# Performance work log

Measured on AMD Instinct MI355X. Metric: run time of the kernel, lower is better.

The kernel has to match this reference:

```python
import jax, jax.numpy as jnp
import numpy as np
import math

D_MODEL = 1024
N_HEADS = 16
HEAD_DIM = D_MODEL // N_HEADS
B = 2
S = 2048

def setup_inputs() -> dict:
    key = jax.random.key(0)
    ks = jax.random.split(key, 5)
    x = jax.random.normal(ks[0], (B, S, D_MODEL), dtype=jnp.float32)
    # causal lower-triangular mask, broadcastable to [B, H, S, S]
    mask = jnp.tril(jnp.ones((S, S), dtype=bool))[None, None, :, :]
    # qkv_proj: Linear(d_model, 3*d_model); out_proj: Linear(d_model, d_model)
    lim_qkv = 1.0 / math.sqrt(D_MODEL)
    Wqkv = jax.random.uniform(ks[1], (D_MODEL, 3 * D_MODEL), minval=-lim_qkv, maxval=lim_qkv, dtype=jnp.float32)
    bqkv = jax.random.uniform(ks[2], (3 * D_MODEL,), minval=-lim_qkv, maxval=lim_qkv, dtype=jnp.float32)
    Wo = jax.random.uniform(ks[3], (D_MODEL, D_MODEL), minval=-lim_qkv, maxval=lim_qkv, dtype=jnp.float32)
    bo = jax.random.uniform(ks[4], (D_MODEL,), minval=-lim_qkv, maxval=lim_qkv, dtype=jnp.float32)
    return {"x": x, "mask": mask, "Wqkv": Wqkv, "bqkv": bqkv, "Wo": Wo, "bo": bo}

def reference(x, mask, Wqkv, bqkv, Wo, bo):
    b, s, d = x.shape
    scale = math.sqrt(HEAD_DIM)
    qkv = x @ Wqkv + bqkv                                   # [b, s, 3d]
    qkv = qkv.reshape(b, s, 3, N_HEADS, HEAD_DIM)
    qkv = jnp.transpose(qkv, (2, 0, 3, 1, 4))               # [3, b, h, s, hd]
    q, k, v = qkv[0], qkv[1], qkv[2]
    scores = jnp.einsum("bhqd,bhkd->bhqk", q, k) / scale    # [b, h, s, s]
    scores = jnp.where(mask, scores, -jnp.inf)
    attn = jax.nn.softmax(scores, axis=-1)                  # dropout inactive (eval)
    out = jnp.einsum("bhqk,bhkd->bhqd", attn, v)            # [b, h, s, hd]
    out = jnp.transpose(out, (0, 2, 1, 3)).reshape(b, s, d)
    return out @ Wo + bo
```

## Files before the change

kernel.cpp:

```cpp
#include <hip/hip_runtime.h>
#include <stdint.h>

typedef __bf16 bf16x8 __attribute__((ext_vector_type(8)));
typedef float  f32x4  __attribute__((ext_vector_type(4)));

__device__ __forceinline__ float bf2f(ushort u) {
    union { uint i; float f; } v; v.i = ((uint)u) << 16; return v.f;
}
__device__ __forceinline__ ushort f2bf(float f) {
    union { uint i; float f; } v; v.f = f;
    uint i = v.i;
    uint r = (i + 0x7fffu + ((i >> 16) & 1u)) >> 16;
    return (ushort)r;
}
__device__ __forceinline__ ushort f2bf_t(float f) {
    union { uint i; float f; } v; v.f = f;
    return (ushort)(v.i >> 16);
}

__device__ __forceinline__ void gld16(const ushort* g, ushort* l) {
    __builtin_amdgcn_global_load_lds((const __attribute__((address_space(1))) uint*)g,
                                     (__attribute__((address_space(3))) uint*)l, 16, 0, 0);
}

#define D_MODEL 1024
#define N_HEADS 16
#define HEAD_DIM 64
#define BATCH 2
#define SEQ 2048
#define M_ROWS (BATCH * SEQ)
#define SCALE_LOG2E 0.18033688f
#define N_ITEMS 768

__global__ __launch_bounds__(256) void cast_f32_bf16(
    const float* __restrict__ in, ushort* __restrict__ out, int n4)
{
    int i = blockIdx.x * 256 + threadIdx.x;
    if (i < n4) {
        float4 v = ((const float4*)in)[i];
        ushort4 o;
        o.x = f2bf(v.x); o.y = f2bf(v.y); o.z = f2bf(v.z); o.w = f2bf(v.w);
        ((ushort4*)out)[i] = o;
    }
}

__global__ __launch_bounds__(256) void transpose_f32_bf16(
    const float* __restrict__ in, ushort* __restrict__ out, int K, int N)
{
    __shared__ float tile[64][65];
    const int k0 = blockIdx.y << 6, n0 = blockIdx.x << 6;
    const int tid = threadIdx.x;
    {
        const int r  = tid >> 4;
        const int c4 = (tid & 15) * 4;
#pragma unroll
        for (int rr = 0; rr < 4; ++rr) {
            int kk = r + rr * 16;
            float4 v = *(const float4*)(in + (size_t)(k0 + kk) * N + n0 + c4);
            tile[kk][c4 + 0] = v.x; tile[kk][c4 + 1] = v.y;
            tile[kk][c4 + 2] = v.z; tile[kk][c4 + 3] = v.w;
        }
    }
    __syncthreads();
    {
        const int nn = tid & 63;
        const int ch = tid >> 6;
#pragma unroll
        for (int cc = 0; cc < 2; ++cc) {
            int k8 = (ch + cc * 4) * 8;
            ushort tmp[8] __attribute__((aligned(16)));
#pragma unroll
            for (int j = 0; j < 8; ++j) tmp[j] = f2bf(tile[k8 + j][nn]);
            *(uint4*)(out + (size_t)(n0 + nn) * K + k0 + k8) = *(const uint4*)tmp;
        }
    }
}

__global__ __launch_bounds__(256) void gemm_bt128(
    const ushort* __restrict__ A, const ushort* __restrict__ Bt,
    const float* __restrict__ bias, float* __restrict__ out,
    ushort* __restrict__ Qb, ushort* __restrict__ Kb, ushort* __restrict__ Vb,
    int M, int N, int K, int mode)
{
    __shared__ ushort As[128 * 32];
    __shared__ ushort Bs[128 * 32];
    const int tid = threadIdx.x, lane = tid & 63, w = tid >> 6;
    const int wr = w >> 1, wc = w & 1;
    const int m0 = blockIdx.y * 128, n0 = blockIdx.x * 128;
    const int quad = lane >> 4, r15 = lane & 15, q8 = quad * 8;

    f32x4 acc[4][4] = {};

    const int cb0 = w * 64;
    const int cb1 = 256 + w * 64;
    const int c0 = cb0 + lane, c1 = cb1 + lane;
    const int row0 = c0 >> 2, sc0 = (c0 & 3) * 8;
    const int row1 = c1 >> 2, sc1 = (c1 & 3) * 8;

    for (int k0 = 0; k0 < K; k0 += 32) {
        gld16(A  + (size_t)(m0 + row0) * K + k0 + sc0, As + cb0 * 8);
        gld16(A  + (size_t)(m0 + row1) * K + k0 + sc1, As + cb1 * 8);
        gld16(Bt + (size_t)(n0 + row0) * K + k0 + sc0, Bs + cb0 * 8);
        gld16(Bt + (size_t)(n0 + row1) * K + k0 + sc1, Bs + cb1 * 8);
        __syncthreads();
        bf16x8 af[4], bfv[4];
#pragma unroll
        for (int mt = 0; mt < 4; ++mt)
            af[mt] = *(const bf16x8*)&As[(wr * 64 + mt * 16 + r15) * 32 + q8];
#pragma unroll
        for (int nt = 0; nt < 4; ++nt)
            bfv[nt] = *(const bf16x8*)&Bs[(wc * 64 + nt * 16 + r15) * 32 + q8];
#pragma unroll
        for (int mt = 0; mt < 4; ++mt)
#pragma unroll
            for (int nt = 0; nt < 4; ++nt)
                acc[mt][nt] = __builtin_amdgcn_mfma_f32_16x16x32_bf16(af[mt], bfv[nt], acc[mt][nt], 0, 0, 0);
        __syncthreads();
    }

    const int q4 = quad * 4;
    float bv[4];
#pragma unroll
    for (int nt = 0; nt < 4; ++nt) bv[nt] = bias[n0 + wc * 64 + nt * 16 + r15];
#pragma unroll
    for (int mt = 0; mt < 4; ++mt) {
#pragma unroll
        for (int nt = 0; nt < 4; ++nt) {
#pragma unroll
            for (int r = 0; r < 4; ++r) {
                int m = m0 + wr * 64 + mt * 16 + q4 + r;
                int n = n0 + wc * 64 + nt * 16 + r15;
                float v = acc[mt][nt][r] + bv[nt];
                if (mode == 0) {
                    int which = n >> 10, nh = n & 1023;
                    int h = nh >> 6, d = nh & 63;
                    int b = m >> 11, s = m & 2047;
                    size_t dst = (((size_t)(b * N_HEADS + h)) * SEQ + s) * HEAD_DIM + d;
                    ushort* p = (which == 0) ? Qb : ((which == 1) ? Kb : Vb);
                    p[dst] = f2bf(v);
                } else {
                    out[(size_t)m * N + n] = v;
                }
            }
        }
    }
}

__global__ __launch_bounds__(512, 4) void attn_mfma(
    const ushort* __restrict__ Q, const ushort* __restrict__ K,
    const ushort* __restrict__ V, ushort* __restrict__ Out,
    float* __restrict__ Opart, float* __restrict__ lpart,
    int* __restrict__ counter)
{
    __shared__ ushort Ks[2][64 * 72];
    __shared__ ushort Vt[2][64 * 72];
    __shared__ ushort Ps[8][16 * 72];
    __shared__ int s_item;

    const int tid  = threadIdx.x;
    const int lane = tid & 63;
    const int w    = tid >> 6;
    const int quad = lane >> 4;
    const int r15  = lane & 15;
    const int q8   = quad * 8;

    const int srow = tid >> 3;
    const int scol = (tid & 7) * 8;
    const int kp = tid & 31;
    const int dg = tid >> 5;

    for (;;) {
        __syncthreads();
        if (tid == 0) s_item = atomicAdd(counter, 1);
        __syncthreads();
        const int item = s_item;
        if (item >= N_ITEMS) break;

        int p, bh, t0, t1, half;
        if (item < 512) {
            p = 15 - (item >> 6);
            half = (item >> 5) & 1;
            bh = item & 31;
            const int hl = p + 1;
            t0 = half * hl; t1 = t0 + hl;
        } else {
            const int j = item - 512;
            p = 7 - (j >> 5);
            bh = j & 31;
            half = -1;
            t0 = 0; t1 = 2 * p + 2;
        }
        const int ntf  = 2 * p + 2;
        const int q0   = p * 128;
        const int wq0  = q0 + w * 16;
        const int tdiag = ntf - 2 + (w >> 2);
        const size_t base = (size_t)bh * SEQ * HEAD_DIM;

        bf16x8 qf[2];
        {
            const ushort* qrow = Q + base + (size_t)(wq0 + r15) * HEAD_DIM;
            qf[0] = *(const bf16x8*)(qrow + q8);
            qf[1] = *(const bf16x8*)(qrow + 32 + q8);
        }

        f32x4 o_acc[4] = {};
        float l_lane[4] = {0.f, 0.f, 0.f, 0.f};

        uint4 kr; uint2 va, vb;
        {
            const int key0 = t0 << 6;
            const ushort* kpt = K + base + (size_t)(key0 + srow) * HEAD_DIM + scol;
            kr = *(const uint4*)kpt;
            const ushort* vpt = V + base + (size_t)(key0 + 2 * kp) * HEAD_DIM + dg * 4;
            va = *(const uint2*)vpt; vb = *(const uint2*)(vpt + HEAD_DIM);
        }
        {
            ushort* ks = &Ks[t0 & 1][0];
            *(uint4*)&ks[srow * 72 + scol] = kr;
            const ushort* ap = (const ushort*)&va;
            const ushort* bp = (const ushort*)&vb;
            uint* vt32 = (uint*)&Vt[t0 & 1][0];
#pragma unroll
            for (int j = 0; j < 4; ++j)
                vt32[(dg * 4 + j) * 36 + kp] = (uint)ap[j] | ((uint)bp[j] << 16);
        }
        if (t0 + 1 < t1) {
            const int key0 = (t0 + 1) << 6;
            const ushort* kpt = K + base + (size_t)(key0 + srow) * HEAD_DIM + scol;
            kr = *(const uint4*)kpt;
            const ushort* vpt = V + base + (size_t)(key0 + 2 * kp) * HEAD_DIM + dg * 4;
            va = *(const uint2*)vpt; vb = *(const uint2*)(vpt + HEAD_DIM);
        }

        for (int t = t0; t < t1; ++t) {
            __syncthreads();
            if (t + 1 < t1) {
                const int b1 = (t + 1) & 1;
                ushort* ks = &Ks[b1][0];
                *(uint4*)&ks[srow * 72 + scol] = kr;
                const ushort* ap = (const ushort*)&va;
                const ushort* bp = (const ushort*)&vb;
                uint* vt32 = (uint*)&Vt[b1][0];
#pragma unroll
                for (int j = 0; j < 4; ++j)
                    vt32[(dg * 4 + j) * 36 + kp] = (uint)ap[j] | ((uint)bp[j] << 16);
            }
            if (t + 2 < t1) {
                const int key2 = (t + 2) << 6;
                const ushort* kpt = K + base + (size_t)(key2 + srow) * HEAD_DIM + scol;
                kr = *(const uint4*)kpt;
                const ushort* vpt = V + base + (size_t)(key2 + 2 * kp) * HEAD_DIM + dg * 4;
                va = *(const uint2*)vpt; vb = *(const uint2*)(vpt + HEAD_DIM);
            }

            const int ntmax = (t < tdiag) ? 4 : ((t == tdiag) ? (w & 3) + 1 : 0);
            if (ntmax == 0) continue;

            const ushort* KsB = &Ks[t & 1][0];
            const ushort* VtB = &Vt[t & 1][0];
            const bool diag = (t == tdiag);

            f32x4 s_acc[4];
#pragma unroll
            for (int nt = 0; nt < 4; ++nt) {
                if (nt >= ntmax) continue;
                f32x4 z = {};
#pragma unroll
                for (int ks = 0; ks < 2; ++ks) {
                    bf16x8 kf = *(const bf16x8*)&KsB[(nt * 16 + r15) * 72 + ks * 32 + q8];
                    z = __builtin_amdgcn_mfma_f32_16x16x32_bf16(qf[ks], kf, z, 0, 0, 0);
                }
                s_acc[nt] = z;
            }
#pragma unroll
            for (int nt = 0; nt < 4; ++nt) {
                if (nt >= ntmax) continue;
#pragma unroll
                for (int j = 0; j < 4; ++j) {
                    float e = exp2f(s_acc[nt][j] * SCALE_LOG2E);
                    if (diag && nt == (w & 3) && r15 > quad * 4 + j) e = 0.f;
                    s_acc[nt][j] = e;
                    l_lane[j] += e;
                }
            }
            ushort* pb = &Ps[w][0];
#pragma unroll
            for (int nt = 0; nt < 4; ++nt)
#pragma unroll
                for (int j = 0; j < 4; ++j)
                    pb[(quad * 4 + j) * 72 + nt * 16 + r15] =
                        (nt < ntmax) ? f2bf_t(s_acc[nt][j]) : (ushort)0;
            bf16x8 pf0 = *(const bf16x8*)&pb[r15 * 72 + q8];
            bf16x8 pf1 = *(const bf16x8*)&pb[r15 * 72 + 32 + q8];

#pragma unroll
            for (int nt = 0; nt < 4; ++nt) {
                const int d0 = nt * 16 + r15;
                bf16x8 vf0 = *(const bf16x8*)&VtB[d0 * 72 + q8];
                bf16x8 vf1 = *(const bf16x8*)&VtB[d0 * 72 + 32 + q8];
                o_acc[nt] = __builtin_amdgcn_mfma_f32_16x16x32_bf16(pf0, vf0, o_acc[nt], 0, 0, 0);
                o_acc[nt] = __builtin_amdgcn_mfma_f32_16x16x32_bf16(pf1, vf1, o_acc[nt], 0, 0, 0);
            }
        }

        float lsum[4];
#pragma unroll
        for (int j = 0; j < 4; ++j) {
            float l = l_lane[j];
            l += __shfl_xor(l, 1);
            l += __shfl_xor(l, 2);
            l += __shfl_xor(l, 4);
            l += __shfl_xor(l, 8);
            lsum[j] = l;
        }
        if (half < 0) {
            const int b = bh >> 4, h = bh & 15;
#pragma unroll
            for (int nt = 0; nt < 4; ++nt) {
#pragma unroll
                for (int j = 0; j < 4; ++j) {
                    int qg = wq0 + quad * 4 + j;
                    float v = o_acc[nt][j] / lsum[j];
                    Out[((size_t)(b * SEQ + qg)) * D_MODEL + h * 64 + nt * 16 + r15] = f2bf(v);
                }
            }
        } else {
            const int qrb = wq0 - 1024;
            float* Ob = Opart + ((size_t)(half * 32 + bh) * 1024) * 64;
#pragma unroll
            for (int nt = 0; nt < 4; ++nt)
#pragma unroll
                for (int j = 0; j < 4; ++j)
                    Ob[(size_t)(qrb + quad * 4 + j) * 64 + nt * 16 + r15] = o_acc[nt][j];
            if (r15 == 0) {
                float* lb = lpart + (size_t)(half * 32 + bh) * 1024;
#pragma unroll
                for (int j = 0; j < 4; ++j)
                    lb[qrb + quad * 4 + j] = lsum[j];
            }
        }
    }
}

__global__ __launch_bounds__(256) void attn_combine(
    const float* __restrict__ Opart, const float* __restrict__ lpart,
    ushort* __restrict__ Out)
{
    const int idx = blockIdx.x * 256 + threadIdx.x;
    const int bh = idx >> 14;
    const int rem = idx & 16383;
    const int qrel = rem >> 4, d4 = (rem & 15) * 4;
    const size_t o0 = ((size_t)bh * 1024 + qrel) * 64 + d4;
    const size_t o1 = ((size_t)(32 + bh) * 1024 + qrel) * 64 + d4;
    float4 a = *(const float4*)(Opart + o0);
    float4 c = *(const float4*)(Opart + o1);
    float l = lpart[bh * 1024 + qrel] + lpart[32 * 1024 + bh * 1024 + qrel];
    float inv = 1.f / l;
    ushort4 r;
    r.x = f2bf((a.x + c.x) * inv);
    r.y = f2bf((a.y + c.y) * inv);
    r.z = f2bf((a.z + c.z) * inv);
    r.w = f2bf((a.w + c.w) * inv);
    const int b = bh >> 4, h = bh & 15;
    *(ushort4*)(Out + ((size_t)(b * SEQ + 1024 + qrel)) * D_MODEL + h * 64 + d4) = r;
}

extern "C" void kernel_launch(void* const* d_in, const int* in_sizes, int n_in,
                              void* d_out, int out_size, void* d_ws, size_t ws_size,
                              hipStream_t stream)
{
    const float* x    = (const float*)d_in[0];
    const float* Wqkv = (const float*)d_in[2];
    const float* bqkv = (const float*)d_in[3];
    const float* Wo   = (const float*)d_in[4];
    const float* bo   = (const float*)d_in[5];
    float* out = (float*)d_out;

    char* ws = (char*)d_ws;
    size_t off = 0;
    ushort* xb    = (ushort*)(ws + off); off += (size_t)M_ROWS * D_MODEL * 2;
    ushort* WqkvT = (ushort*)(ws + off); off += (size_t)3 * D_MODEL * D_MODEL * 2;
    ushort* WoT   = (ushort*)(ws + off); off += (size_t)D_MODEL * D_MODEL * 2;
    const size_t qkv_elems = (size_t)BATCH * N_HEADS * SEQ * HEAD_DIM;
    ushort* Qb = (ushort*)(ws + off); off += qkv_elems * 2;
    ushort* Kb = (ushort*)(ws + off); off += qkv_elems * 2;
    ushort* Vb = (ushort*)(ws + off); off += qkv_elems * 2;
    ushort* attn_out = (ushort*)(ws + off); off += (size_t)M_ROWS * D_MODEL * 2;
    float* Opart = (float*)(ws + off); off += (size_t)2 * 32 * 1024 * 64 * 4;
    float* lpart = (float*)(ws + off); off += (size_t)2 * 32 * 1024 * 4;
    int* counter = (int*)(ws + off); off += 256;

    hipMemsetAsync(counter, 0, 4, stream);

    {
        int n4 = M_ROWS * D_MODEL / 4;
        cast_f32_bf16<<<(n4 + 255) / 256, 256, 0, stream>>>(x, xb, n4);
    }

    transpose_f32_bf16<<<dim3(3 * D_MODEL / 64, D_MODEL / 64), 256, 0, stream>>>(Wqkv, WqkvT, D_MODEL, 3 * D_MODEL);
    transpose_f32_bf16<<<dim3(D_MODEL / 64, D_MODEL / 64), 256, 0, stream>>>(Wo, WoT, D_MODEL, D_MODEL);

    gemm_bt128<<<dim3(3 * D_MODEL / 128, M_ROWS / 128), 256, 0, stream>>>(
        xb, WqkvT, bqkv, nullptr, Qb, Kb, Vb, M_ROWS, 3 * D_MODEL, D_MODEL, 0);

    attn_mfma<<<512, 512, 0, stream>>>(Qb, Kb, Vb, attn_out, Opart, lpart, counter);

    attn_combine<<<2048, 256, 0, stream>>>(Opart, lpart, attn_out);

    gemm_bt128<<<dim3(D_MODEL / 128, M_ROWS / 128), 256, 0, stream>>>(
        attn_out, WoT, bo, out, nullptr, nullptr, nullptr, M_ROWS, D_MODEL, D_MODEL, 1);
}
```

Before: 247.1 us.

## Fuse prep kernels and fold split-KV combine into output projection GEMM

Merges the x cast and both weight transposes into one launch, specialises the QKV GEMM, and removes the attn_combine kernel. The output GEMM now combines the two partial attention results and normalises them while loading its A tile for the second half of each sequence, using 64-row tiles. This saves kernel launches and one write-then-read of the combined attention output. In exchange, the heavy tiles do scalar float loads and conversions in the GEMM inner loop, and each Opart row is reread by every N-block, so that load becomes redundant.

Result: faster. 240.8 us (-2.6%).

```diff
diff --git a/kernel.cpp b/kernel.cpp
--- a/kernel.cpp
+++ b/kernel.cpp
@@ -32,24 +32,35 @@
 #define SCALE_LOG2E 0.18033688f
 #define N_ITEMS 768
 
-__global__ __launch_bounds__(256) void cast_f32_bf16(
-    const float* __restrict__ in, ushort* __restrict__ out, int n4)
+__global__ __launch_bounds__(256) void prep_fused(
+    const float* __restrict__ x, ushort* __restrict__ xb,
+    const float* __restrict__ Wqkv, ushort* __restrict__ WqkvT,
+    const float* __restrict__ Wo, ushort* __restrict__ WoT)
 {
-    int i = blockIdx.x * 256 + threadIdx.x;
-    if (i < n4) {
-        float4 v = ((const float4*)in)[i];
+    __shared__ float tile[64][65];
+    const int blk = blockIdx.x;
+    const int tid = threadIdx.x;
+
+    if (blk < 4096) {
+        int i = blk * 256 + tid;
+        float4 v = ((const float4*)x)[i];
         ushort4 o;
         o.x = f2bf(v.x); o.y = f2bf(v.y); o.z = f2bf(v.z); o.w = f2bf(v.w);
-        ((ushort4*)out)[i] = o;
-    }
-}
-
-__global__ __launch_bounds__(256) void transpose_f32_bf16(
-    const float* __restrict__ in, ushort* __restrict__ out, int K, int N)
-{
-    __shared__ float tile[64][65];
-    const int k0 = blockIdx.y << 6, n0 = blockIdx.x << 6;
-    const int tid = threadIdx.x;
+        ((ushort4*)xb)[i] = o;
+        return;
+    }
+
+    const float* in; ushort* out; int K, N, bx, by;
+    if (blk < 4096 + 768) {
+        int j = blk - 4096;
+        in = Wqkv; out = WqkvT; K = 1024; N = 3072;
+        bx = j % 48; by = j / 48;
+    } else {
+        int j = blk - 4864;
+        in = Wo; out = WoT; K = 1024; N = 1024;
+        bx = j & 15; by = j >> 4;
+    }
+    const int k0 = by << 6, n0 = bx << 6;
     {
         const int r  = tid >> 4;
         const int c4 = (tid & 15) * 4;
@@ -76,11 +87,10 @@
     }
 }
 
-__global__ __launch_bounds__(256) void gemm_bt128(
+__global__ __launch_bounds__(256) void gemm_qkv(
     const ushort* __restrict__ A, const ushort* __restrict__ Bt,
-    const float* __restrict__ bias, float* __restrict__ out,
-    ushort* __restrict__ Qb, ushort* __restrict__ Kb, ushort* __restrict__ Vb,
-    int M, int N, int K, int mode)
+    const float* __restrict__ bias,
+    ushort* __restrict__ Qb, ushort* __restrict__ Kb, ushort* __restrict__ Vb)
 {
     __shared__ ushort As[128 * 32];
     __shared__ ushort Bs[128 * 32];
@@ -88,6 +98,7 @@
     const int wr = w >> 1, wc = w & 1;
     const int m0 = blockIdx.y * 128, n0 = blockIdx.x * 128;
     const int quad = lane >> 4, r15 = lane & 15, q8 = quad * 8;
+    const int K = D_MODEL;
 
     f32x4 acc[4][4] = {};
 
@@ -131,16 +142,12 @@
                 int m = m0 + wr * 64 + mt * 16 + q4 + r;
                 int n = n0 + wc * 64 + nt * 16 + r15;
                 float v = acc[mt][nt][r] + bv[nt];
-                if (mode == 0) {
-                    int which = n >> 10, nh = n & 1023;
-                    int h = nh >> 6, d = nh & 63;
-                    int b = m >> 11, s = m & 2047;
-                    size_t dst = (((size_t)(b * N_HEADS + h)) * SEQ + s) * HEAD_DIM + d;
-                    ushort* p = (which == 0) ? Qb : ((which == 1) ? Kb : Vb);
-                    p[dst] = f2bf(v);
-                } else {
-                    out[(size_t)m * N + n] = v;
-                }
+                int which = n >> 10, nh = n & 1023;
+                int h = nh >> 6, d = nh & 63;
+                int b = m >> 11, s = m & 2047;
+                size_t dst = (((size_t)(b * N_HEADS + h)) * SEQ + s) * HEAD_DIM + d;
+                ushort* p = (which == 0) ? Qb : ((which == 1) ? Kb : Vb);
+                p[dst] = f2bf(v);
             }
         }
     }
@@ -342,27 +349,98 @@
     }
 }
 
-__global__ __launch_bounds__(256) void attn_combine(
+__global__ __launch_bounds__(256) void gemm_out(
+    const ushort* __restrict__ A,
     const float* __restrict__ Opart, const float* __restrict__ lpart,
-    ushort* __restrict__ Out)
+    const ushort* __restrict__ Bt,
+    const float* __restrict__ bias, float* __restrict__ out)
 {
-    const int idx = blockIdx.x * 256 + threadIdx.x;
-    const int bh = idx >> 14;
-    const int rem = idx & 16383;
-    const int qrel = rem >> 4, d4 = (rem & 15) * 4;
-    const size_t o0 = ((size_t)bh * 1024 + qrel) * 64 + d4;
-    const size_t o1 = ((size_t)(32 + bh) * 1024 + qrel) * 64 + d4;
-    float4 a = *(const float4*)(Opart + o0);
-    float4 c = *(const float4*)(Opart + o1);
-    float l = lpart[bh * 1024 + qrel] + lpart[32 * 1024 + bh * 1024 + qrel];
-    float inv = 1.f / l;
-    ushort4 r;
-    r.x = f2bf((a.x + c.x) * inv);
-    r.y = f2bf((a.y + c.y) * inv);
-    r.z = f2bf((a.z + c.z) * inv);
-    r.w = f2bf((a.w + c.w) * inv);
-    const int b = bh >> 4, h = bh & 15;
-    *(ushort4*)(Out + ((size_t)(b * SEQ + 1024 + qrel)) * D_MODEL + h * 64 + d4) = r;
+    __shared__ ushort As[64 * 32];
+    __shared__ ushort Bs[128 * 32];
+    const int tid = threadIdx.x, lane = tid & 63, w = tid >> 6;
+    const int wr = w >> 1, wc = w & 1;
+    const int m0 = blockIdx.y * 64, n0 = blockIdx.x * 128;
+    const int quad = lane >> 4, r15 = lane & 15, q8 = quad * 8;
+    const bool heavy = ((m0 >> 10) & 1) != 0;
+
+    f32x4 acc[2][4] = {};
+
+    const int ca = w * 64 + lane;
+    const int rowa = ca >> 2, sca = (ca & 3) * 8;
+    const int hrow = tid >> 2, hc8 = (tid & 3) * 8;
+    const int m_h = m0 + hrow;
+    const int qrel = (m_h & 2047) - 1024;
+    const int b_h = m_h >> 11;
+    float inv_l = 0.f;
+    if (heavy) {
+    }
+    const int cb0 = w * 64, cb1 = 256 + w * 64;
+    const int c0 = cb0 + lane, c1 = cb1 + lane;
+    const int rowb0 = c0 >> 2, scb0 = (c0 & 3) * 8;
+    const int rowb1 = c1 >> 2, scb1 = (c1 & 3) * 8;
+
+    int cur_h = -1;
+    for (int k0 = 0; k0 < D_MODEL; k0 += 32) {
+        if (heavy) {
+            const int h = k0 >> 6;
+            const int bh = b_h * 16 + h;
+            if (h != cur_h) {
+                float l = lpart[bh * 1024 + qrel] + lpart[32768 + bh * 1024 + qrel];
+                inv_l = 1.f / l;
+                cur_h = h;
+            }
+            const int d = (k0 & 63) + hc8;
+            const float* p0 = Opart + ((size_t)bh * 1024 + qrel) * 64 + d;
+            const float* p1 = p0 + (size_t)32 * 1024 * 64;
+            float4 a0 = *(const float4*)p0, a1 = *(const float4*)(p0 + 4);
+            float4 c0v = *(const float4*)p1, c1v = *(const float4*)(p1 + 4);
+            ushort tmp[8] __attribute__((aligned(16)));
+            tmp[0] = f2bf((a0.x + c0v.x) * inv_l);
+            tmp[1] = f2bf((a0.y + c0v.y) * inv_l);
+            tmp[2] = f2bf((a0.z + c0v.z) * inv_l);
+            tmp[3] = f2bf((a0.w + c0v.w) * inv_l);
+            tmp[4] = f2bf((a1.x + c1v.x) * inv_l);
+            tmp[5] = f2bf((a1.y + c1v.y) * inv_l);
+            tmp[6] = f2bf((a1.z + c1v.z) * inv_l);
+            tmp[7] = f2bf((a1.w + c1v.w) * inv_l);
+            *(uint4*)&As[hrow * 32 + hc8] = *(const uint4*)tmp;
+        } else {
+            gld16(A + (size_t)(m0 + rowa) * D_MODEL + k0 + sca, As + cb0 * 8);
+        }
+        gld16(Bt + (size_t)(n0 + rowb0) * D_MODEL + k0 + scb0, Bs + cb0 * 8);
+        gld16(Bt + (size_t)(n0 + rowb1) * D_MODEL + k0 + scb1, Bs + cb1 * 8);
+        __syncthreads();
+        bf16x8 af[2], bfv[4];
+#pragma unroll
+        for (int mt = 0; mt < 2; ++mt)
+            af[mt] = *(const bf16x8*)&As[(wr * 32 + mt * 16 + r15) * 32 + q8];
+#pragma unroll
+        for (int nt = 0; nt < 4; ++nt)
+            bfv[nt] = *(const bf16x8*)&Bs[(wc * 64 + nt * 16 + r15) * 32 + q8];
+#pragma unroll
+        for (int mt = 0; mt < 2; ++mt)
+#pragma unroll
+            for (int nt = 0; nt < 4; ++nt)
+                acc[mt][nt] = __builtin_amdgcn_mfma_f32_16x16x32_bf16(af[mt], bfv[nt], acc[mt][nt], 0, 0, 0);
+        __syncthreads();
+    }
+
+    const int q4 = quad * 4;
+    float bv[4];
+#pragma unroll
+    for (int nt = 0; nt < 4; ++nt) bv[nt] = bias[n0 + wc * 64 + nt * 16 + r15];
+#pragma unroll
+    for (int mt = 0; mt < 2; ++mt) {
+#pragma unroll
+        for (int nt = 0; nt < 4; ++nt) {
+#pragma unroll
+            for (int r = 0; r < 4; ++r) {
+                int m = m0 + wr * 32 + mt * 16 + q4 + r;
+                int n = n0 + wc * 64 + nt * 16 + r15;
+                out[(size_t)m * D_MODEL + n] = acc[mt][nt][r] + bv[nt];
+            }
+        }
+    }
 }
 
 extern "C" void kernel_launch(void* const* d_in, const int* in_sizes, int n_in,
@@ -392,21 +470,13 @@
 
     hipMemsetAsync(counter, 0, 4, stream);
 
-    {
-        int n4 = M_ROWS * D_MODEL / 4;
-        cast_f32_bf16<<<(n4 + 255) / 256, 256, 0, stream>>>(x, xb, n4);
-    }
-
-    transpose_f32_bf16<<<dim3(3 * D_MODEL / 64, D_MODEL / 64), 256, 0, stream>>>(Wqkv, WqkvT, D_MODEL, 3 * D_MODEL);
-    transpose_f32_bf16<<<dim3(D_MODEL / 64, D_MODEL / 64), 256, 0, stream>>>(Wo, WoT, D_MODEL, D_MODEL);
-
-    gemm_bt128<<<dim3(3 * D_MODEL / 128, M_ROWS / 128), 256, 0, stream>>>(
-        xb, WqkvT, bqkv, nullptr, Qb, Kb, Vb, M_ROWS, 3 * D_MODEL, D_MODEL, 0);
+    prep_fused<<<5120, 256, 0, stream>>>(x, xb, Wqkv, WqkvT, Wo, WoT);
+
+    gemm_qkv<<<dim3(3 * D_MODEL / 128, M_ROWS / 128), 256, 0, stream>>>(
+        xb, WqkvT, bqkv, Qb, Kb, Vb);
 
     attn_mfma<<<512, 512, 0, stream>>>(Qb, Kb, Vb, attn_out, Opart, lpart, counter);
 
-    attn_combine<<<2048, 256, 0, stream>>>(Opart, lpart, attn_out);
-
-    gemm_bt128<<<dim3(D_MODEL / 128, M_ROWS / 128), 256, 0, stream>>>(
-        attn_out, WoT, bo, out, nullptr, nullptr, nullptr, M_ROWS, D_MODEL, D_MODEL, 1);
-}
+    gemm_out<<<dim3(D_MODEL / 128, M_ROWS / 64), 256, 0, stream>>>(
+        attn_out, Opart, lpart, WoT, bo, out);
+}
```

## Fuse whole attention pipeline into one persistent kernel with grid barriers

Applied to the files above, without the earlier changes.

Replaces the seven separate launches (cast, two transposes, QKV GEMM, attention, combine, output GEMM) with a single persistent 256-block kernel whose phases are separated by atomic-counter grid barriers. QKV is now written row-major to one buffer instead of being scattered per head, and attention is statically balanced by pairing a long and a short query block per block, which removes the split-half partial outputs and the combine pass. Launch overhead and the extra partial-output traffic go away, but the GEMMs now run with smaller tiles over only 256 blocks. The grid barriers rely on every block being co-resident and add spin-wait stalls between phases.

After: 362.7 us. 1.47x slower.

```diff
diff --git a/kernel.cpp b/kernel.cpp
--- a/kernel.cpp
+++ b/kernel.cpp
@@ -4,9 +4,6 @@
 typedef __bf16 bf16x8 __attribute__((ext_vector_type(8)));
 typedef float  f32x4  __attribute__((ext_vector_type(4)));
 
-__device__ __forceinline__ float bf2f(ushort u) {
-    union { uint i; float f; } v; v.i = ((uint)u) << 16; return v.f;
-}
 __device__ __forceinline__ ushort f2bf(float f) {
     union { uint i; float f; } v; v.f = f;
     uint i = v.i;
@@ -29,340 +26,320 @@
 #define BATCH 2
 #define SEQ 2048
 #define M_ROWS (BATCH * SEQ)
+#define QKV_W  3072
 #define SCALE_LOG2E 0.18033688f
-#define N_ITEMS 768
-
-__global__ __launch_bounds__(256) void cast_f32_bf16(
-    const float* __restrict__ in, ushort* __restrict__ out, int n4)
+#define NBLK 256
+
+__device__ __forceinline__ void grid_barrier(int* cnt, int target, int tid) {
+    __syncthreads();
+    if (tid == 0) {
+        __threadfence();
+        atomicAdd(cnt, 1);
+        while (__hip_atomic_load(cnt, __ATOMIC_ACQUIRE, __HIP_MEMORY_SCOPE_AGENT) < target)
+            __builtin_amdgcn_s_sleep(2);
+        __threadfence();
+    }
+    __syncthreads();
+}
+
+__global__ __launch_bounds__(512, 4) void fused_all(
+    const float* __restrict__ x,    ushort* __restrict__ xb,
+    const float* __restrict__ Wqkv, ushort* __restrict__ WqkvT,
+    const float* __restrict__ Wo,   ushort* __restrict__ WoT,
+    const float* __restrict__ bqkv, ushort* __restrict__ xqkv,
+    ushort* __restrict__ aout, const float* __restrict__ bo,
+    float* __restrict__ out, int* __restrict__ cnt)
 {
-    int i = blockIdx.x * 256 + threadIdx.x;
-    if (i < n4) {
-        float4 v = ((const float4*)in)[i];
-        ushort4 o;
-        o.x = f2bf(v.x); o.y = f2bf(v.y); o.z = f2bf(v.z); o.w = f2bf(v.w);
-        ((ushort4*)out)[i] = o;
-    }
-}
-
-__global__ __launch_bounds__(256) void transpose_f32_bf16(
-    const float* __restrict__ in, ushort* __restrict__ out, int K, int N)
-{
-    __shared__ float tile[64][65];
-    const int k0 = blockIdx.y << 6, n0 = blockIdx.x << 6;
-    const int tid = threadIdx.x;
-    {
-        const int r  = tid >> 4;
-        const int c4 = (tid & 15) * 4;
-#pragma unroll
-        for (int rr = 0; rr < 4; ++rr) {
-            int kk = r + rr * 16;
-            float4 v = *(const float4*)(in + (size_t)(k0 + kk) * N + n0 + c4);
-            tile[kk][c4 + 0] = v.x; tile[kk][c4 + 1] = v.y;
-            tile[kk][c4 + 2] = v.z; tile[kk][c4 + 3] = v.w;
-        }
-    }
-    __syncthreads();
-    {
-        const int nn = tid & 63;
-        const int ch = tid >> 6;
-#pragma unroll
-        for (int cc = 0; cc < 2; ++cc) {
-            int k8 = (ch + cc * 4) * 8;
-            ushort tmp[8] __attribute__((aligned(16)));
-#pragma unroll
-            for (int j = 0; j < 8; ++j) tmp[j] = f2bf(tile[k8 + j][nn]);
-            *(uint4*)(out + (size_t)(n0 + nn) * K + k0 + k8) = *(const uint4*)tmp;
-        }
-    }
-}
-
-__global__ __launch_bounds__(256) void gemm_bt128(
-    const ushort* __restrict__ A, const ushort* __restrict__ Bt,
-    const float* __restrict__ bias, float* __restrict__ out,
-    ushort* __restrict__ Qb, ushort* __restrict__ Kb, ushort* __restrict__ Vb,
-    int M, int N, int K, int mode)
-{
-    __shared__ ushort As[128 * 32];
-    __shared__ ushort Bs[128 * 32];
-    const int tid = threadIdx.x, lane = tid & 63, w = tid >> 6;
-    const int wr = w >> 1, wc = w & 1;
-    const int m0 = blockIdx.y * 128, n0 = blockIdx.x * 128;
-    const int quad = lane >> 4, r15 = lane & 15, q8 = quad * 8;
-
-    f32x4 acc[4][4] = {};
-
-    const int cb0 = w * 64;
-    const int cb1 = 256 + w * 64;
-    const int c0 = cb0 + lane, c1 = cb1 + lane;
-    const int row0 = c0 >> 2, sc0 = (c0 & 3) * 8;
-    const int row1 = c1 >> 2, sc1 = (c1 & 3) * 8;
-
-    for (int k0 = 0; k0 < K; k0 += 32) {
-        gld16(A  + (size_t)(m0 + row0) * K + k0 + sc0, As + cb0 * 8);
-        gld16(A  + (size_t)(m0 + row1) * K + k0 + sc1, As + cb1 * 8);
-        gld16(Bt + (size_t)(n0 + row0) * K + k0 + sc0, Bs + cb0 * 8);
-        gld16(Bt + (size_t)(n0 + row1) * K + k0 + sc1, Bs + cb1 * 8);
-        __syncthreads();
-        bf16x8 af[4], bfv[4];
-#pragma unroll
-        for (int mt = 0; mt < 4; ++mt)
-            af[mt] = *(const bf16x8*)&As[(wr * 64 + mt * 16 + r15) * 32 + q8];
-#pragma unroll
-        for (int nt = 0; nt < 4; ++nt)
-            bfv[nt] = *(const bf16x8*)&Bs[(wc * 64 + nt * 16 + r15) * 32 + q8];
-#pragma unroll
-        for (int mt = 0; mt < 4; ++mt)
-#pragma unroll
-            for (int nt = 0; nt < 4; ++nt)
-                acc[mt][nt] = __builtin_amdgcn_mfma_f32_16x16x32_bf16(af[mt], bfv[nt], acc[mt][nt], 0, 0, 0);
-        __syncthreads();
-    }
-
-    const int q4 = quad * 4;
-    float bv[4];
-#pragma unroll
-    for (int nt = 0; nt < 4; ++nt) bv[nt] = bias[n0 + wc * 64 + nt * 16 + r15];
-#pragma unroll
-    for (int mt = 0; mt < 4; ++mt) {
-#pragma unroll
-        for (int nt = 0; nt < 4; ++nt) {
-#pragma unroll
-            for (int r = 0; r < 4; ++r) {
-                int m = m0 + wr * 64 + mt * 16 + q4 + r;
-                int n = n0 + wc * 64 + nt * 16 + r15;
-                float v = acc[mt][nt][r] + bv[nt];
-                if (mode == 0) {
-                    int which = n >> 10, nh = n & 1023;
-                    int h = nh >> 6, d = nh & 63;
-                    int b = m >> 11, s = m & 2047;
-                    size_t dst = (((size_t)(b * N_HEADS + h)) * SEQ + s) * HEAD_DIM + d;
-                    ushort* p = (which == 0) ? Qb : ((which == 1) ? Kb : Vb);
-                    p[dst] = f2bf(v);
-                } else {
-                    out[(size_t)m * N + n] = v;
-                }
-            }
-        }
-    }
-}
-
-__global__ __launch_bounds__(512, 4) void attn_mfma(
-    const ushort* __restrict__ Q, const ushort* __restrict__ K,
-    const ushort* __restrict__ V, ushort* __restrict__ Out,
-    float* __restrict__ Opart, float* __restrict__ lpart,
-    int* __restrict__ counter)
-{
-    __shared__ ushort Ks[2][64 * 72];
-    __shared__ ushort Vt[2][64 * 72];
-    __shared__ ushort Ps[8][16 * 72];
-    __shared__ int s_item;
+    __shared__ ushort smem[27648] __attribute__((aligned(16)));
 
     const int tid  = threadIdx.x;
+    const int bi   = blockIdx.x;
     const int lane = tid & 63;
     const int w    = tid >> 6;
     const int quad = lane >> 4;
     const int r15  = lane & 15;
     const int q8   = quad * 8;
 
-    const int srow = tid >> 3;
-    const int scol = (tid & 7) * 8;
-    const int kp = tid & 31;
-    const int dg = tid >> 5;
-
-    for (;;) {
-        __syncthreads();
-        if (tid == 0) s_item = atomicAdd(counter, 1);
-        __syncthreads();
-        const int item = s_item;
-        if (item >= N_ITEMS) break;
-
-        int p, bh, t0, t1, half;
-        if (item < 512) {
-            p = 15 - (item >> 6);
-            half = (item >> 5) & 1;
-            bh = item & 31;
-            const int hl = p + 1;
-            t0 = half * hl; t1 = t0 + hl;
-        } else {
-            const int j = item - 512;
-            p = 7 - (j >> 5);
-            bh = j & 31;
-            half = -1;
-            t0 = 0; t1 = 2 * p + 2;
-        }
-        const int ntf  = 2 * p + 2;
-        const int q0   = p * 128;
-        const int wq0  = q0 + w * 16;
-        const int tdiag = ntf - 2 + (w >> 2);
-        const size_t base = (size_t)bh * SEQ * HEAD_DIM;
-
-        bf16x8 qf[2];
-        {
-            const ushort* qrow = Q + base + (size_t)(wq0 + r15) * HEAD_DIM;
-            qf[0] = *(const bf16x8*)(qrow + q8);
-            qf[1] = *(const bf16x8*)(qrow + 32 + q8);
-        }
-
-        f32x4 o_acc[4] = {};
-        float l_lane[4] = {0.f, 0.f, 0.f, 0.f};
-
-        uint4 kr; uint2 va, vb;
-        {
-            const int key0 = t0 << 6;
-            const ushort* kpt = K + base + (size_t)(key0 + srow) * HEAD_DIM + scol;
-            kr = *(const uint4*)kpt;
-            const ushort* vpt = V + base + (size_t)(key0 + 2 * kp) * HEAD_DIM + dg * 4;
-            va = *(const uint2*)vpt; vb = *(const uint2*)(vpt + HEAD_DIM);
-        }
-        {
-            ushort* ks = &Ks[t0 & 1][0];
-            *(uint4*)&ks[srow * 72 + scol] = kr;
-            const ushort* ap = (const ushort*)&va;
-            const ushort* bp = (const ushort*)&vb;
-            uint* vt32 = (uint*)&Vt[t0 & 1][0];
-#pragma unroll
-            for (int j = 0; j < 4; ++j)
-                vt32[(dg * 4 + j) * 36 + kp] = (uint)ap[j] | ((uint)bp[j] << 16);
-        }
-        if (t0 + 1 < t1) {
-            const int key0 = (t0 + 1) << 6;
-            const ushort* kpt = K + base + (size_t)(key0 + srow) * HEAD_DIM + scol;
-            kr = *(const uint4*)kpt;
-            const ushort* vpt = V + base + (size_t)(key0 + 2 * kp) * HEAD_DIM + dg * 4;
-            va = *(const uint2*)vpt; vb = *(const uint2*)(vpt + HEAD_DIM);
-        }
-
-        for (int t = t0; t < t1; ++t) {
+    {
+#pragma unroll
+        for (int k = 0; k < 8; ++k) {
+            int i = k * 131072 + bi * 512 + tid;
+            float4 v = ((const float4*)x)[i];
+            ushort4 o;
+            o.x = f2bf(v.x); o.y = f2bf(v.y); o.z = f2bf(v.z); o.w = f2bf(v.w);
+            ((ushort4*)xb)[i] = o;
+        }
+        float (*tile)[65] = (float(*)[65])(void*)smem;
+        for (int jj = 0; jj < 4; ++jj) {
+            const int job = bi * 4 + jj;
+            const float* in; ushort* outp; int Nd, bx, by;
+            if (job < 768) { in = Wqkv; outp = WqkvT; Nd = QKV_W;   bx = job % 48;         by = job / 48; }
+            else           { in = Wo;   outp = WoT;   Nd = D_MODEL; bx = (job - 768) & 15; by = (job - 768) >> 4; }
+            const int k0 = by << 6, n0 = bx << 6;
             __syncthreads();
-            if (t + 1 < t1) {
-                const int b1 = (t + 1) & 1;
-                ushort* ks = &Ks[b1][0];
-                *(uint4*)&ks[srow * 72 + scol] = kr;
+            {
+                const int r = tid >> 3, c8 = (tid & 7) * 8;
+                const float* src = in + (size_t)(k0 + r) * Nd + n0 + c8;
+                float4 v0 = *(const float4*)src;
+                float4 v1 = *(const float4*)(src + 4);
+                tile[r][c8 + 0] = v0.x; tile[r][c8 + 1] = v0.y;
+                tile[r][c8 + 2] = v0.z; tile[r][c8 + 3] = v0.w;
+                tile[r][c8 + 4] = v1.x; tile[r][c8 + 5] = v1.y;
+                tile[r][c8 + 6] = v1.z; tile[r][c8 + 7] = v1.w;
+            }
+            __syncthreads();
+            {
+                const int nn = tid & 63, k8 = (tid >> 6) * 8;
+                ushort tmp[8] __attribute__((aligned(16)));
+#pragma unroll
+                for (int j = 0; j < 8; ++j) tmp[j] = f2bf(tile[k8 + j][nn]);
+                *(uint4*)(outp + (size_t)(n0 + nn) * D_MODEL + k0 + k8) = *(const uint4*)tmp;
+            }
+        }
+    }
+    grid_barrier(cnt, NBLK, tid);
+
+    {
+        ushort* As = smem;
+        ushort* Bs = smem + 4096;
+        const int wr = w >> 1, wc = w & 1;
+        const int crow = tid >> 2, ccol8 = (tid & 3) * 8;
+
+        for (int ti = bi; ti < 768; ti += NBLK) {
+            const int bx = ti % 24, by = ti / 24;
+            const int m0 = by * 128, n0 = bx * 128;
+            f32x4 acc[2][4] = {};
+
+            for (int k0 = 0; k0 < D_MODEL; k0 += 32) {
+                gld16(xb    + (size_t)(m0 + crow) * D_MODEL + k0 + ccol8, As + w * 512);
+                gld16(WqkvT + (size_t)(n0 + crow) * D_MODEL + k0 + ccol8, Bs + w * 512);
+                __syncthreads();
+                bf16x8 af[2], bfv[4];
+#pragma unroll
+                for (int mt = 0; mt < 2; ++mt)
+                    af[mt] = *(const bf16x8*)&As[(wr * 32 + mt * 16 + r15) * 32 + q8];
+#pragma unroll
+                for (int nt = 0; nt < 4; ++nt)
+                    bfv[nt] = *(const bf16x8*)&Bs[(wc * 64 + nt * 16 + r15) * 32 + q8];
+#pragma unroll
+                for (int mt = 0; mt < 2; ++mt)
+#pragma unroll
+                    for (int nt = 0; nt < 4; ++nt)
+                        acc[mt][nt] = __builtin_amdgcn_mfma_f32_16x16x32_bf16(af[mt], bfv[nt], acc[mt][nt], 0, 0, 0);
+                __syncthreads();
+            }
+
+            float bv[4];
+#pragma unroll
+            for (int nt = 0; nt < 4; ++nt) bv[nt] = bqkv[n0 + wc * 64 + nt * 16 + r15];
+#pragma unroll
+            for (int mt = 0; mt < 2; ++mt)
+#pragma unroll
+                for (int nt = 0; nt < 4; ++nt)
+#pragma unroll
+                    for (int r = 0; r < 4; ++r) {
+                        int m = m0 + wr * 32 + mt * 16 + quad * 4 + r;
+                        int n = n0 + wc * 64 + nt * 16 + r15;
+                        xqkv[(size_t)m * QKV_W + n] = f2bf(acc[mt][nt][r] + bv[nt]);
+                    }
+        }
+    }
+    grid_barrier(cnt, 2 * NBLK, tid);
+
+    {
+        ushort* KsA = smem;
+        ushort* VtA = smem + 9216;
+        ushort* Ps  = smem + 18432;
+
+        const int pp = bi >> 5;
+        const int bh = bi & 31;
+        const int b = bh >> 4, h = bh & 15;
+        const int brow = b * SEQ;
+        const int qcol = h * 64, kcol = D_MODEL + h * 64, vcol = 2 * D_MODEL + h * 64;
+
+        const int srow = tid >> 3;
+        const int scol = (tid & 7) * 8;
+        const int kp = tid & 31;
+        const int dg = tid >> 5;
+
+        for (int it = 0; it < 2; ++it) {
+            const int p = (it == 0) ? (15 - pp) : pp;
+            const int t1   = 2 * p + 2;
+            const int q0   = p * 128;
+            const int wq0  = q0 + w * 16;
+            const int tdiag = t1 - 2 + (w >> 2);
+
+            __syncthreads();
+
+            bf16x8 qf[2];
+            {
+                const ushort* qrow = xqkv + (size_t)(brow + wq0 + r15) * QKV_W + qcol;
+                qf[0] = *(const bf16x8*)(qrow + q8);
+                qf[1] = *(const bf16x8*)(qrow + 32 + q8);
+            }
+
+            f32x4 o_acc[4] = {};
+            float l_lane[4] = {0.f, 0.f, 0.f, 0.f};
+
+            uint4 kr; uint2 va, vb;
+            {
+                const ushort* kpt = xqkv + (size_t)(brow + srow) * QKV_W + kcol + scol;
+                kr = *(const uint4*)kpt;
+                const ushort* vpt = xqkv + (size_t)(brow + 2 * kp) * QKV_W + vcol + dg * 4;
+                va = *(const uint2*)vpt; vb = *(const uint2*)(vpt + QKV_W);
+            }
+            {
+                *(uint4*)&KsA[srow * 72 + scol] = kr;
                 const ushort* ap = (const ushort*)&va;
                 const ushort* bp = (const ushort*)&vb;
-                uint* vt32 = (uint*)&Vt[b1][0];
+                uint* vt32 = (uint*)VtA;
 #pragma unroll
                 for (int j = 0; j < 4; ++j)
                     vt32[(dg * 4 + j) * 36 + kp] = (uint)ap[j] | ((uint)bp[j] << 16);
             }
-            if (t + 2 < t1) {
-                const int key2 = (t + 2) << 6;
-                const ushort* kpt = K + base + (size_t)(key2 + srow) * HEAD_DIM + scol;
+            if (1 < t1) {
+                const ushort* kpt = xqkv + (size_t)(brow + 64 + srow) * QKV_W + kcol + scol;
                 kr = *(const uint4*)kpt;
-                const ushort* vpt = V + base + (size_t)(key2 + 2 * kp) * HEAD_DIM + dg * 4;
-                va = *(const uint2*)vpt; vb = *(const uint2*)(vpt + HEAD_DIM);
-            }
-
-            const int ntmax = (t < tdiag) ? 4 : ((t == tdiag) ? (w & 3) + 1 : 0);
-            if (ntmax == 0) continue;
-
-            const ushort* KsB = &Ks[t & 1][0];
-            const ushort* VtB = &Vt[t & 1][0];
-            const bool diag = (t == tdiag);
-
-            f32x4 s_acc[4];
-#pragma unroll
-            for (int nt = 0; nt < 4; ++nt) {
-                if (nt >= ntmax) continue;
-                f32x4 z = {};
-#pragma unroll
-                for (int ks = 0; ks < 2; ++ks) {
-                    bf16x8 kf = *(const bf16x8*)&KsB[(nt * 16 + r15) * 72 + ks * 32 + q8];
-                    z = __builtin_amdgcn_mfma_f32_16x16x32_bf16(qf[ks], kf, z, 0, 0, 0);
-                }
-                s_acc[nt] = z;
-            }
-#pragma unroll
-            for (int nt = 0; nt < 4; ++nt) {
-                if (nt >= ntmax) continue;
-#pragma unroll
-                for (int j = 0; j < 4; ++j) {
-                    float e = exp2f(s_acc[nt][j] * SCALE_LOG2E);
-                    if (diag && nt == (w & 3) && r15 > quad * 4 + j) e = 0.f;
-                    s_acc[nt][j] = e;
-                    l_lane[j] += e;
-                }
-            }
-            ushort* pb = &Ps[w][0];
+                const ushort* vpt = xqkv + (size_t)(brow + 64 + 2 * kp) * QKV_W + vcol + dg * 4;
+                va = *(const uint2*)vpt; vb = *(const uint2*)(vpt + QKV_W);
+            }
+
+            for (int t = 0; t < t1; ++t) {
+                __syncthreads();
+                if (t + 1 < t1) {
+                    const int b1 = (t + 1) & 1;
+                    ushort* ks = KsA + b1 * 4608;
+                    *(uint4*)&ks[srow * 72 + scol] = kr;
+                    const ushort* ap = (const ushort*)&va;
+                    const ushort* bp = (const ushort*)&vb;
+                    uint* vt32 = (uint*)(VtA + b1 * 4608);
+#pragma unroll
+                    for (int j = 0; j < 4; ++j)
+                        vt32[(dg * 4 + j) * 36 + kp] = (uint)ap[j] | ((uint)bp[j] << 16);
+                }
+                if (t + 2 < t1) {
+                    const int key2 = (t + 2) << 6;
+                    const ushort* kpt = xqkv + (size_t)(brow + key2 + srow) * QKV_W + kcol + scol;
+                    kr = *(const uint4*)kpt;
+                    const ushort* vpt = xqkv + (size_t)(brow + key2 + 2 * kp) * QKV_W + vcol + dg * 4;
+                    va = *(const uint2*)vpt; vb = *(const uint2*)(vpt + QKV_W);
+                }
+
+                const int ntmax = (t < tdiag) ? 4 : ((t == tdiag) ? (w & 3) + 1 : 0);
+                if (ntmax == 0) continue;
+
+                const ushort* KsB = KsA + (t & 1) * 4608;
+                const ushort* VtB = VtA + (t & 1) * 4608;
+                const bool diag = (t == tdiag);
+
+                f32x4 s_acc[4];
+#pragma unroll
+                for (int nt = 0; nt < 4; ++nt) {
+                    if (nt >= ntmax) continue;
+                    f32x4 z = {};
+#pragma unroll
+                    for (int ks = 0; ks < 2; ++ks) {
+                        bf16x8 kf = *(const bf16x8*)&KsB[(nt * 16 + r15) * 72 + ks * 32 + q8];
+                        z = __builtin_amdgcn_mfma_f32_16x16x32_bf16(qf[ks], kf, z, 0, 0, 0);
+                    }
+                    s_acc[nt] = z;
+                }
+#pragma unroll
+                for (int nt = 0; nt < 4; ++nt) {
+                    if (nt >= ntmax) continue;
+#pragma unroll
+                    for (int j = 0; j < 4; ++j) {
+                        float e = exp2f(s_acc[nt][j] * SCALE_LOG2E);
+                        if (diag && nt == (w & 3) && r15 > quad * 4 + j) e = 0.f;
+                        s_acc[nt][j] = e;
+                        l_lane[j] += e;
+                    }
+                }
+                ushort* pb = Ps + w * (16 * 72);
+#pragma unroll
+                for (int nt = 0; nt < 4; ++nt)
+#pragma unroll
+                    for (int j = 0; j < 4; ++j)
+                        pb[(quad * 4 + j) * 72 + nt * 16 + r15] =
+                            (nt < ntmax) ? f2bf_t(s_acc[nt][j]) : (ushort)0;
+                bf16x8 pf0 = *(const bf16x8*)&pb[r15 * 72 + q8];
+                bf16x8 pf1 = *(const bf16x8*)&pb[r15 * 72 + 32 + q8];
+
+#pragma unroll
+                for (int nt = 0; nt < 4; ++nt) {
+                    const int d0 = nt * 16 + r15;
+                    bf16x8 vf0 = *(const bf16x8*)&VtB[d0 * 72 + q8];
+                    bf16x8 vf1 = *(const bf16x8*)&VtB[d0 * 72 + 32 + q8];
+                    o_acc[nt] = __builtin_amdgcn_mfma_f32_16x16x32_bf16(pf0, vf0, o_acc[nt], 0, 0, 0);
+                    o_acc[nt] = __builtin_amdgcn_mfma_f32_16x16x32_bf16(pf1, vf1, o_acc[nt], 0, 0, 0);
+                }
+            }
+
+            float lsum[4];
+#pragma unroll
+            for (int j = 0; j < 4; ++j) {
+                float l = l_lane[j];
+                l += __shfl_xor(l, 1);
+                l += __shfl_xor(l, 2);
+                l += __shfl_xor(l, 4);
+                l += __shfl_xor(l, 8);
+                lsum[j] = l;
+            }
 #pragma unroll
             for (int nt = 0; nt < 4; ++nt)
-#pragma unroll
-                for (int j = 0; j < 4; ++j)
-                    pb[(quad * 4 + j) * 72 + nt * 16 + r15] =
-                        (nt < ntmax) ? f2bf_t(s_acc[nt][j]) : (ushort)0;
-            bf16x8 pf0 = *(const bf16x8*)&pb[r15 * 72 + q8];
-            bf16x8 pf1 = *(const bf16x8*)&pb[r15 * 72 + 32 + q8];
-
-#pragma unroll
-            for (int nt = 0; nt < 4; ++nt) {
-                const int d0 = nt * 16 + r15;
-                bf16x8 vf0 = *(const bf16x8*)&VtB[d0 * 72 + q8];
-                bf16x8 vf1 = *(const bf16x8*)&VtB[d0 * 72 + 32 + q8];
-                o_acc[nt] = __builtin_amdgcn_mfma_f32_16x16x32_bf16(pf0, vf0, o_acc[nt], 0, 0, 0);
-                o_acc[nt] = __builtin_amdgcn_mfma_f32_16x16x32_bf16(pf1, vf1, o_acc[nt], 0, 0, 0);
-            }
-        }
-
-        float lsum[4];
-#pragma unroll
-        for (int j = 0; j < 4; ++j) {
-            float l = l_lane[j];
-            l += __shfl_xor(l, 1);
-            l += __shfl_xor(l, 2);
-            l += __shfl_xor(l, 4);
-            l += __shfl_xor(l, 8);
-            lsum[j] = l;
-        }
-        if (half < 0) {
-            const int b = bh >> 4, h = bh & 15;
-#pragma unroll
-            for (int nt = 0; nt < 4; ++nt) {
 #pragma unroll
                 for (int j = 0; j < 4; ++j) {
                     int qg = wq0 + quad * 4 + j;
                     float v = o_acc[nt][j] / lsum[j];
-                    Out[((size_t)(b * SEQ + qg)) * D_MODEL + h * 64 + nt * 16 + r15] = f2bf(v);
-                }
-            }
-        } else {
-            const int qrb = wq0 - 1024;
-            float* Ob = Opart + ((size_t)(half * 32 + bh) * 1024) * 64;
-#pragma unroll
-            for (int nt = 0; nt < 4; ++nt)
-#pragma unroll
-                for (int j = 0; j < 4; ++j)
-                    Ob[(size_t)(qrb + quad * 4 + j) * 64 + nt * 16 + r15] = o_acc[nt][j];
-            if (r15 == 0) {
-                float* lb = lpart + (size_t)(half * 32 + bh) * 1024;
-#pragma unroll
-                for (int j = 0; j < 4; ++j)
-                    lb[qrb + quad * 4 + j] = lsum[j];
-            }
-        }
-    }
-}
-
-__global__ __launch_bounds__(256) void attn_combine(
-    const float* __restrict__ Opart, const float* __restrict__ lpart,
-    ushort* __restrict__ Out)
-{
-    const int idx = blockIdx.x * 256 + threadIdx.x;
-    const int bh = idx >> 14;
-    const int rem = idx & 16383;
-    const int qrel = rem >> 4, d4 = (rem & 15) * 4;
-    const size_t o0 = ((size_t)bh * 1024 + qrel) * 64 + d4;
-    const size_t o1 = ((size_t)(32 + bh) * 1024 + qrel) * 64 + d4;
-    float4 a = *(const float4*)(Opart + o0);
-    float4 c = *(const float4*)(Opart + o1);
-    float l = lpart[bh * 1024 + qrel] + lpart[32 * 1024 + bh * 1024 + qrel];
-    float inv = 1.f / l;
-    ushort4 r;
-    r.x = f2bf((a.x + c.x) * inv);
-    r.y = f2bf((a.y + c.y) * inv);
-    r.z = f2bf((a.z + c.z) * inv);
-    r.w = f2bf((a.w + c.w) * inv);
-    const int b = bh >> 4, h = bh & 15;
-    *(ushort4*)(Out + ((size_t)(b * SEQ + 1024 + qrel)) * D_MODEL + h * 64 + d4) = r;
+                    aout[(size_t)(brow + qg) * D_MODEL + h * 64 + nt * 16 + r15] = f2bf(v);
+                }
+        }
+    }
+    grid_barrier(cnt, 3 * NBLK, tid);
+
+    {
+        ushort* As = smem;
+        ushort* Bs = smem + 2048;
+        const int wr = w >> 1;
+        const int wc = w & 1;
+        const int crow = tid >> 2, ccol8 = (tid & 3) * 8;
+        const int arow = (tid & 255) >> 2, acol8 = (tid & 3) * 8;
+
+        __syncthreads();
+
+        for (int ti = bi * 2; ti < bi * 2 + 2; ++ti) {
+            const int by = ti >> 3, bx = ti & 7;
+            const int m0 = by * 64, n0 = bx * 128;
+            f32x4 acc[4] = {};
+
+            for (int k0 = 0; k0 < D_MODEL; k0 += 32) {
+                if (w < 4)
+                    gld16(aout + (size_t)(m0 + arow) * D_MODEL + k0 + acol8, As + w * 512);
+                gld16(WoT + (size_t)(n0 + crow) * D_MODEL + k0 + ccol8, Bs + w * 512);
+                __syncthreads();
+                bf16x8 af = *(const bf16x8*)&As[(wr * 16 + r15) * 32 + q8];
+                bf16x8 bfv[4];
+#pragma unroll
+                for (int nt = 0; nt < 4; ++nt)
+                    bfv[nt] = *(const bf16x8*)&Bs[(wc * 64 + nt * 16 + r15) * 32 + q8];
+#pragma unroll
+                for (int nt = 0; nt < 4; ++nt)
+                    acc[nt] = __builtin_amdgcn_mfma_f32_16x16x32_bf16(af, bfv[nt], acc[nt], 0, 0, 0);
+                __syncthreads();
+            }
+
+#pragma unroll
+            for (int nt = 0; nt < 4; ++nt) {
+                float bvn = bo[n0 + wc * 64 + nt * 16 + r15];
+#pragma unroll
+                for (int r = 0; r < 4; ++r) {
+                    int m = m0 + wr * 16 + quad * 4 + r;
+                    int n = n0 + wc * 64 + nt * 16 + r15;
+                    out[(size_t)m * D_MODEL + n] = acc[nt][r] + bvn;
+                }
+            }
+        }
+    }
 }
 
 extern "C" void kernel_launch(void* const* d_in, const int* in_sizes, int n_in,
@@ -379,34 +356,14 @@
     char* ws = (char*)d_ws;
     size_t off = 0;
     ushort* xb    = (ushort*)(ws + off); off += (size_t)M_ROWS * D_MODEL * 2;
-    ushort* WqkvT = (ushort*)(ws + off); off += (size_t)3 * D_MODEL * D_MODEL * 2;
+    ushort* WqkvT = (ushort*)(ws + off); off += (size_t)QKV_W * D_MODEL * 2;
     ushort* WoT   = (ushort*)(ws + off); off += (size_t)D_MODEL * D_MODEL * 2;
-    const size_t qkv_elems = (size_t)BATCH * N_HEADS * SEQ * HEAD_DIM;
-    ushort* Qb = (ushort*)(ws + off); off += qkv_elems * 2;
-    ushort* Kb = (ushort*)(ws + off); off += qkv_elems * 2;
-    ushort* Vb = (ushort*)(ws + off); off += qkv_elems * 2;
-    ushort* attn_out = (ushort*)(ws + off); off += (size_t)M_ROWS * D_MODEL * 2;
-    float* Opart = (float*)(ws + off); off += (size_t)2 * 32 * 1024 * 64 * 4;
-    float* lpart = (float*)(ws + off); off += (size_t)2 * 32 * 1024 * 4;
-    int* counter = (int*)(ws + off); off += 256;
-
-    hipMemsetAsync(counter, 0, 4, stream);
-
-    {
-        int n4 = M_ROWS * D_MODEL / 4;
-        cast_f32_bf16<<<(n4 + 255) / 256, 256, 0, stream>>>(x, xb, n4);
-    }
-
-    transpose_f32_bf16<<<dim3(3 * D_MODEL / 64, D_MODEL / 64), 256, 0, stream>>>(Wqkv, WqkvT, D_MODEL, 3 * D_MODEL);
-    transpose_f32_bf16<<<dim3(D_MODEL / 64, D_MODEL / 64), 256, 0, stream>>>(Wo, WoT, D_MODEL, D_MODEL);
-
-    gemm_bt128<<<dim3(3 * D_MODEL / 128, M_ROWS / 128), 256, 0, stream>>>(
-        xb, WqkvT, bqkv, nullptr, Qb, Kb, Vb, M_ROWS, 3 * D_MODEL, D_MODEL, 0);
-
-    attn_mfma<<<512, 512, 0, stream>>>(Qb, Kb, Vb, attn_out, Opart, lpart, counter);
-
-    attn_combine<<<2048, 256, 0, stream>>>(Opart, lpart, attn_out);
-
-    gemm_bt128<<<dim3(D_MODEL / 128, M_ROWS / 128), 256, 0, stream>>>(
-        attn_out, WoT, bo, out, nullptr, nullptr, nullptr, M_ROWS, D_MODEL, D_MODEL, 1);
-}
+    ushort* xqkv  = (ushort*)(ws + off); off += (size_t)M_ROWS * QKV_W * 2;
+    ushort* aout  = (ushort*)(ws + off); off += (size_t)M_ROWS * D_MODEL * 2;
+    int* cnt      = (int*)(ws + off);    off += 256;
+
+    hipMemsetAsync(cnt, 0, 4, stream);
+
+    fused_all<<<NBLK, 512, 0, stream>>>(x, xb, Wqkv, WqkvT, Wo, WoT,
+                                        bqkv, xqkv, aout, bo, out, cnt);
+}
```
